# Optimization experiments

Measured on AMD Instinct MI355X. Metric: run time of the kernel, lower is better.

## Reference

```python
import jax, jax.numpy as jnp
from jax import lax
import numpy as np


def _conv3x3(x, w, b):
    # x: [B,C,H,W], w: [O,I,3,3] (OIHW), SAME padding, stride 1
    y = lax.conv_general_dilated(x, w, window_strides=(1, 1), padding='SAME',
                                 dimension_numbers=('NCHW', 'OIHW', 'NCHW'))
    return y + b[None, :, None, None]


def setup_inputs() -> dict:
    key = jax.random.key(0)
    ks = jax.random.split(key, 9)
    B, C, H, W = 4, 64, 64, 64
    wscale = 1.0 / np.sqrt(C * 9)  # keep conv outputs / attention logits sane
    x = jax.random.normal(ks[0], (B, C, H, W), dtype=jnp.float32)
    wq = jax.random.normal(ks[1], (C, C, 3, 3), dtype=jnp.float32) * wscale
    bq = jax.random.normal(ks[2], (C,), dtype=jnp.float32) * 0.1
    wk = jax.random.normal(ks[3], (C, C, 3, 3), dtype=jnp.float32) * wscale
    bk = jax.random.normal(ks[4], (C,), dtype=jnp.float32) * 0.1
    wv = jax.random.normal(ks[5], (C, C, 3, 3), dtype=jnp.float32) * wscale
    bv = jax.random.normal(ks[6], (C,), dtype=jnp.float32) * 0.1
    pos_gamma = jax.random.normal(ks[7], (1,), dtype=jnp.float32)
    chan_gamma = jax.random.normal(ks[8], (1,), dtype=jnp.float32)
    return {'x': x, 'wq': wq, 'bq': bq, 'wk': wk, 'bk': bk, 'wv': wv, 'bv': bv,
            'pos_gamma': pos_gamma, 'chan_gamma': chan_gamma}


def reference(x, wq, bq, wk, bk, wv, bv, pos_gamma, chan_gamma):
    B, C, H, W = x.shape
    N = H * W
    # position (spatial) self-attention over N = H*W locations
    q = _conv3x3(x, wq, bq).reshape(B, C, N)
    k = _conv3x3(x, wk, bk).reshape(B, C, N)
    v = _conv3x3(x, wv, bv).reshape(B, C, N)
    # attn[b,i,j] = softmax_j( sum_c q[b,c,i] * k[b,c,j] )
    pos_attn = jax.nn.softmax(jnp.einsum('bci,bcj->bij', q, k), axis=-1)
    # pos_out[b,c,j] = sum_i v[b,c,i] * attn[b,i,j]  (matches torch.bmm(v, attn))
    pos = jnp.einsum('bci,bij->bcj', v, pos_attn).reshape(B, C, H, W)
    pos_out = pos_gamma * pos + x
    # channel self-attention over C channels (x is its own q/k/v)
    xf = x.reshape(B, C, N)
    chan_attn = jax.nn.softmax(jnp.einsum('bcn,bdn->bcd', xf, xf), axis=-1)
    chan = jnp.einsum('bcd,bdn->bcn', chan_attn, xf).reshape(B, C, H, W)
    chan_out = chan_gamma * chan + x
    return pos_out + chan_out
```

## Files before the change

kernel.cpp:

```cpp
#include <hip/hip_runtime.h>

#define OFF_XV2   65536u
#define OFF_GP    589824u
#define OFF_Q2    1048576u
#define OFF_K2    2097152u
#define OFF_V2    3145728u
#define OFF_X2    3670016u
#define OFF_WT    4194304u
#define OFF_INVL  4452352u
#define OFF_A     4730880u
#define WS_FLOATS 4747264u

typedef short s8v __attribute__((ext_vector_type(8)));
typedef float f16v __attribute__((ext_vector_type(16)));

#define MFMA32(a, b, c) __builtin_amdgcn_mfma_f32_32x32x16_bf16((a), (b), (c), 0, 0, 0)

__device__ __forceinline__ unsigned short bf16_rne(float f) {
    union { float f; unsigned int u; } v; v.f = f;
    unsigned int r = v.u + 0x7FFFu + ((v.u >> 16) & 1u);
    return (unsigned short)(r >> 16);
}
__device__ __forceinline__ float bf2f(unsigned short h) {
    union { unsigned int u; float f; } t; t.u = ((unsigned int)h) << 16;
    return t.f;
}
__device__ __forceinline__ void split2(float f, unsigned short& h, unsigned short& l) {
    unsigned short hh = bf16_rne(f);
    h = hh;
    l = bf16_rne(f - bf2f(hh));
}
__device__ __forceinline__ unsigned int cvtpk(float lo, float hi) {
    unsigned int r;
    asm("v_cvt_pk_bf16_f32 %0, %1, %2" : "=v"(r) : "v"(lo), "v"(hi));
    return r;
}
__device__ __forceinline__ void pl32swap(unsigned int& a, unsigned int& b) {
    asm volatile("v_permlane32_swap_b32 %0, %1" : "+v"(a), "+v"(b));
}
__device__ __forceinline__ s8v mk8(unsigned int w0, unsigned int w1,
                                   unsigned int w2, unsigned int w3) {
    union { unsigned int u[4]; s8v v; } t;
    t.u[0] = w0; t.u[1] = w1; t.u[2] = w2; t.u[3] = w3;
    return t.v;
}
__device__ __forceinline__ f16v zero16() {
    f16v z;
#pragma unroll
    for (int i = 0; i < 16; ++i) z[i] = 0.0f;
    return z;
}


__global__ void k_wtrans(const float* __restrict__ wq, const float* __restrict__ wk,
                         const float* __restrict__ wv, unsigned short* __restrict__ wf) {
    int t = blockIdx.x * 256 + threadIdx.x;
    int f = t >> 9, pos = t & 511;
    int lane = pos >> 3, e = pos & 7;
    int oc = f & 1, kst = (f >> 1) & 3;
    int ct = f >> 3;
    int tap = ct % 9, conv = ct / 9;
    int o = oc * 32 + (lane & 31);
    int ci = kst * 16 + (lane >> 5) * 8 + e;
    const float* w = (conv == 0) ? wq : (conv == 1) ? wk : wv;
    float v = w[(o * 64 + ci) * 9 + tap];
    unsigned short hh, ll;
    split2(v, hh, ll);
    wf[(f * 2 + 0) * 512 + pos] = hh;
    wf[(f * 2 + 1) * 512 + pos] = ll;
}

__global__ __launch_bounds__(256) void k_xpack(const float* __restrict__ x,
                                               unsigned short* __restrict__ X2,
                                               unsigned short* __restrict__ XV2) {
    int gid = blockIdx.x * 256 + threadIdx.x;
    int b = gid >> 16;
    int c = (gid >> 10) & 63;
    int n4 = (gid & 1023) * 4;
    float4 v = *(const float4*)(x + (size_t)(b * 64 + c) * 4096 + n4);
    unsigned short hv[4] = {bf16_rne(v.x), bf16_rne(v.y), bf16_rne(v.z), bf16_rne(v.w)};
    int kst = c >> 4, e = c & 7, hb = (c >> 3) & 1;
#pragma unroll
    for (int u = 0; u < 4; ++u) {
        int n = n4 + u;
        int nch = n >> 5, lane = (n & 31) + 32 * hb;
        X2[(size_t)((b * 128 + nch) * 4 + kst) * 512 + lane * 8 + e] = hv[u];
    }
    int ich = n4 >> 5, ksub = (n4 >> 4) & 1, cb = c >> 5;
    int lane2 = (c & 31) + 32 * ((n4 >> 3) & 1);
    size_t xi = (size_t)(((b * 128 + ich) * 2 + ksub) * 2 + cb) * 512 + lane2 * 8 + (n4 & 7);
    unsigned long long w = (unsigned long long)hv[0]
                         | ((unsigned long long)hv[1] << 16)
                         | ((unsigned long long)hv[2] << 32)
                         | ((unsigned long long)hv[3] << 48);
    *(unsigned long long*)(XV2 + xi) = w;
}

__global__ __launch_bounds__(384) void k_conv(
        const float* __restrict__ x, const unsigned short* __restrict__ wf,
        const float* __restrict__ bq, const float* __restrict__ bk, const float* __restrict__ bv,
        unsigned short* __restrict__ Q2, unsigned short* __restrict__ K2,
        unsigned short* __restrict__ V2) {
    int nb = blockIdx.x;
    int b = blockIdx.y;
    int h = nb >> 1, w0 = (nb & 1) * 32;

    __shared__ unsigned short xwh[6528];
    __shared__ unsigned short xwl[6528];

    int tid = threadIdx.x;
    for (int idx = tid; idx < 6528; idx += 384) {
        int W = idx % 34;
        int c = (idx / 34) & 63;
        int dy = idx / (34 * 64);
        int hs = h + dy - 1, wi = w0 + W - 1;
        float v = 0.0f;
        if (hs >= 0 && hs < 64 && wi >= 0 && wi < 64)
            v = x[((b * 64 + c) * 64 + hs) * 64 + wi];
        unsigned short hh_, ll_;
        split2(v, hh_, ll_);
        int row = dy * 34 + W;
        int byt = row * 128 + c * 2;
        int swz = byt ^ ((row & 7) << 4);
        *(unsigned short*)((char*)xwh + swz) = hh_;
        *(unsigned short*)((char*)xwl + swz) = ll_;
    }
    __syncthreads();

    int lane = tid & 63, wv = tid >> 6;
    int conv = wv >> 1, oc = wv & 1;
    int hh = lane >> 5, l31 = lane & 31;

    const float* bias = (conv == 0) ? bq : (conv == 1) ? bk : bv;
    f16v D;
    if (conv < 2) {
#pragma unroll
        for (int r = 0; r < 16; ++r)
            D[r] = bias[oc * 32 + (r & 3) + 8 * (r >> 2) + 4 * hh];
    } else {
        float bvv = bias[oc * 32 + l31];
#pragma unroll
        for (int r = 0; r < 16; ++r) D[r] = bvv;
    }

#pragma unroll
    for (int tap = 0; tap < 9; ++tap) {
        int dy = tap / 3, dx = tap % 3;
#pragma unroll
        for (int kst = 0; kst < 4; ++kst) {
            int f = ((conv * 9 + tap) * 4 + kst) * 2 + oc;
            s8v Wh = *(const s8v*)(wf + (f * 2 + 0) * 512 + lane * 8);
            s8v Wl = *(const s8v*)(wf + (f * 2 + 1) * 512 + lane * 8);
            int row = dy * 34 + dx + l31;
            int byt = row * 128 + kst * 32 + hh * 16;
            int swz = byt ^ ((row & 7) << 4);
            s8v Xh = *(const s8v*)((const char*)xwh + swz);
            s8v Xl = *(const s8v*)((const char*)xwl + swz);
            if (conv < 2) {
                D = MFMA32(Wh, Xh, D);
                D = MFMA32(Wh, Xl, D);
                D = MFMA32(Wl, Xh, D);
            } else {
                D = MFMA32(Xh, Wh, D);
                D = MFMA32(Xl, Wh, D);
                D = MFMA32(Xh, Wl, D);
            }
        }
    }

    if (conv < 2) {
        unsigned short sh[16], sl[16];
#pragma unroll
        for (int r = 0; r < 16; ++r) split2(D[r], sh[r], sl[r]);
        unsigned int ah0 = sh[0] | ((unsigned int)sh[1] << 16), ah1 = sh[2] | ((unsigned int)sh[3] << 16);
        unsigned int ah2 = sh[4] | ((unsigned int)sh[5] << 16), ah3 = sh[6] | ((unsigned int)sh[7] << 16);
        pl32swap(ah0, ah2); pl32swap(ah1, ah3);
        s8v F0h = mk8(ah0, ah1, ah2, ah3);
        unsigned int al0 = sl[0] | ((unsigned int)sl[1] << 16), al1 = sl[2] | ((unsigned int)sl[3] << 16);
        unsigned int al2 = sl[4] | ((unsigned int)sl[5] << 16), al3 = sl[6] | ((unsigned int)sl[7] << 16);
        pl32swap(al0, al2); pl32swap(al1, al3);
        s8v F0l = mk8(al0, al1, al2, al3);
        unsigned int bh0 = sh[8] | ((unsigned int)sh[9] << 16), bh1 = sh[10] | ((unsigned int)sh[11] << 16);
        unsigned int bh2 = sh[12] | ((unsigned int)sh[13] << 16), bh3 = sh[14] | ((unsigned int)sh[15] << 16);
        pl32swap(bh0, bh2); pl32swap(bh1, bh3);
        s8v F1h = mk8(bh0, bh1, bh2, bh3);
        unsigned int bl0 = sl[8] | ((unsigned int)sl[9] << 16), bl1 = sl[10] | ((unsigned int)sl[11] << 16);
        unsigned int bl2 = sl[12] | ((unsigned int)sl[13] << 16), bl3 = sl[14] | ((unsigned int)sl[15] << 16);
        pl32swap(bl0, bl2); pl32swap(bl1, bl3);
        s8v F1l = mk8(bl0, bl1, bl2, bl3);
        unsigned short* dst = (conv == 0) ? Q2 : K2;
        size_t b0 = (size_t)(((b * 128 + nb) * 4 + oc * 2 + 0) * 2) * 512 + lane * 8;
        size_t b1 = (size_t)(((b * 128 + nb) * 4 + oc * 2 + 1) * 2) * 512 + lane * 8;
        *(s8v*)(dst + b0) = F0h;
        *(s8v*)(dst + b0 + 512) = F0l;
        *(s8v*)(dst + b1) = F1h;
        *(s8v*)(dst + b1 + 512) = F1l;
    } else {
        unsigned int a0 = cvtpk(D[0], D[1]),  a1 = cvtpk(D[2], D[3]);
        unsigned int a2 = cvtpk(D[4], D[5]),  a3 = cvtpk(D[6], D[7]);
        pl32swap(a0, a2); pl32swap(a1, a3);
        s8v F0h = mk8(a0, a1, a2, a3);
        unsigned int b0w = cvtpk(D[8], D[9]),  b1w = cvtpk(D[10], D[11]);
        unsigned int b2w = cvtpk(D[12], D[13]), b3w = cvtpk(D[14], D[15]);
        pl32swap(b0w, b2w); pl32swap(b1w, b3w);
        s8v F1h = mk8(b0w, b1w, b2w, b3w);
        size_t v0 = (size_t)(((b * 128 + nb) * 2 + 0) * 2 + oc) * 512 + lane * 8;
        size_t v1 = (size_t)(((b * 128 + nb) * 2 + 1) * 2 + oc) * 512 + lane * 8;
        *(s8v*)(V2 + v0) = F0h;
        *(s8v*)(V2 + v1) = F1h;
    }
}

__global__ __launch_bounds__(256) void k_gram(const unsigned short* __restrict__ XV2,
                                              float* __restrict__ Gp) {
    int kp = blockIdx.x, b = blockIdx.y;
    int tid = threadIdx.x, lane = tid & 63, wv = tid >> 6;
    int cb1 = wv & 1, cb2 = wv >> 1;
    f16v G = zero16();
#pragma unroll
    for (int t = 0; t < 8; ++t) {
        int ich = kp * 8 + t;
        const unsigned short* base = XV2 + (size_t)(b * 128 + ich) * 2048 + lane * 8;
        s8v a0 = *(const s8v*)(base + (0 * 2 + cb1) * 512);
        s8v b0 = *(const s8v*)(base + (0 * 2 + cb2) * 512);
        s8v a1 = *(const s8v*)(base + (1 * 2 + cb1) * 512);
        s8v b1 = *(const s8v*)(base + (1 * 2 + cb2) * 512);
        G = MFMA32(a0, b0, G);
        G = MFMA32(a1, b1, G);
    }
    int hh = lane >> 5, l31 = lane & 31;
#pragma unroll
    for (int r = 0; r < 16; ++r) {
        int cc = cb1 * 32 + (r & 3) + 8 * (r >> 2) + 4 * hh;
        int dd = cb2 * 32 + l31;
        Gp[(size_t)(kp * 4 + b) * 4096 + cc * 64 + dd] = G[r];
    }
}

__global__ void k_asm(const float* __restrict__ Gp, unsigned short* __restrict__ A2) {
    int row = blockIdx.x;
    int d = threadIdx.x;
    int b = row >> 6, c = row & 63;
    float g = 0.0f;
#pragma unroll
    for (int p = 0; p < 16; ++p) g += Gp[(size_t)(p * 4 + b) * 4096 + c * 64 + d];
    float mx = g;
    for (int off = 32; off >= 1; off >>= 1) mx = fmaxf(mx, __shfl_xor(mx, off, 64));
    float e = __expf(g - mx);
    float s = e;
    for (int off = 32; off >= 1; off >>= 1) s += __shfl_xor(s, off, 64);
    float a = e / s;
    int cb = c >> 5, kst = d >> 4;
    int lane2 = (c & 31) + 32 * ((d >> 3) & 1);
    A2[(size_t)((b * 2 + cb) * 4 + kst) * 512 + lane2 * 8 + (d & 7)] = bf16_rne(a);
}

__global__ __launch_bounds__(1024) void k_pass1(
        const unsigned short* __restrict__ Q2, const unsigned short* __restrict__ K2,
        float* __restrict__ invl) {
    int flat = blockIdx.x;
    int xcd = flat & 7;
    int b = xcd >> 1;
    int ich = (xcd & 1) * 64 + (flat >> 3);
    int tid = threadIdx.x, lane = tid & 63, wv = tid >> 6;

    __shared__ float lsum[16][32];

    const unsigned short* qp = Q2 + (size_t)(b * 128 + ich) * 4096 + lane * 8;
    s8v qf0 = *(const s8v*)(qp);
    s8v qf1 = *(const s8v*)(qp + 512);
    s8v qf2 = *(const s8v*)(qp + 1024);
    s8v qf3 = *(const s8v*)(qp + 1536);
    s8v qf4 = *(const s8v*)(qp + 2048);
    s8v qf5 = *(const s8v*)(qp + 2560);
    s8v qf6 = *(const s8v*)(qp + 3072);
    s8v qf7 = *(const s8v*)(qp + 3584);

    float la0 = 0.f, la1 = 0.f;
#pragma unroll 1
    for (int t = 0; t < 8; ++t) {
        int jch = wv * 8 + t;
        const unsigned short* kp = K2 + (size_t)(b * 128 + jch) * 4096 + lane * 8;
        s8v kf0 = *(const s8v*)(kp);
        s8v kf1 = *(const s8v*)(kp + 512);
        s8v kf2 = *(const s8v*)(kp + 1024);
        s8v kf3 = *(const s8v*)(kp + 1536);
        s8v kf4 = *(const s8v*)(kp + 2048);
        s8v kf5 = *(const s8v*)(kp + 2560);
        s8v kf6 = *(const s8v*)(kp + 3072);
        s8v kf7 = *(const s8v*)(kp + 3584);
        f16v Sa = zero16(), Sb = zero16();
        Sa = MFMA32(kf0, qf0, Sa);
        Sa = MFMA32(kf0, qf1, Sa);
        Sa = MFMA32(kf1, qf0, Sa);
        Sa = MFMA32(kf2, qf2, Sa);
        Sa = MFMA32(kf2, qf3, Sa);
        Sa = MFMA32(kf3, qf2, Sa);
        Sb = MFMA32(kf4, qf4, Sb);
        Sb = MFMA32(kf4, qf5, Sb);
        Sb = MFMA32(kf5, qf4, Sb);
        Sb = MFMA32(kf6, qf6, Sb);
        Sb = MFMA32(kf6, qf7, Sb);
        Sb = MFMA32(kf7, qf6, Sb);
#pragma unroll
        for (int r = 0; r < 8; ++r) la0 += __expf(Sa[r] + Sb[r]);
#pragma unroll
        for (int r = 8; r < 16; ++r) la1 += __expf(Sa[r] + Sb[r]);
    }
    float lacc = la0 + la1;
    lacc += __shfl_xor(lacc, 32);
    if (lane < 32) lsum[wv][lane] = lacc;
    __syncthreads();
    if (tid < 32) {
        float s = 0.f;
#pragma unroll
        for (int p = 0; p < 16; ++p) s += lsum[p][tid];
        invl[b * 4096 + ich * 32 + tid] = 1.0f / s;
    }
}

__global__ __launch_bounds__(256) void k_vnorm(
        unsigned short* __restrict__ V2, const float* __restrict__ invl) {
    int u = blockIdx.x * 256 + threadIdx.x;
    int lane = u & 63, ksub = (u >> 7) & 1;
    int ich = (u >> 8) & 127, b = u >> 15;
    int n0 = ich * 32 + ksub * 16 + (lane >> 5) * 8;
    size_t base = (size_t)u * 8;
    s8v vh = *(s8v*)(V2 + base);
    float4 iv0 = *(const float4*)(invl + b * 4096 + n0);
    float4 iv1 = *(const float4*)(invl + b * 4096 + n0 + 4);
    float ivv[8] = {iv0.x, iv0.y, iv0.z, iv0.w, iv1.x, iv1.y, iv1.z, iv1.w};
    s8v o;
#pragma unroll
    for (int e = 0; e < 8; ++e)
        o[e] = (short)bf16_rne(bf2f((unsigned short)vh[e]) * ivv[e]);
    *(s8v*)(V2 + base) = o;
}

__global__ __launch_bounds__(512) void k_pass2(
        const unsigned short* __restrict__ Q2, const unsigned short* __restrict__ K2,
        const unsigned short* __restrict__ V2, const unsigned short* __restrict__ X2,
        const unsigned short* __restrict__ A2, const float* __restrict__ x,
        const float* __restrict__ pg, const float* __restrict__ cg,
        float* __restrict__ out) {
    int flat = blockIdx.x;
    int xcd = flat & 7;
    int b = xcd >> 1;
    int jt = (xcd & 1) * 64 + (flat >> 3);
    int tid = threadIdx.x, lane = tid & 63, wv = tid >> 6;

    __shared__ float rlds[4][64][32];

    const unsigned short* kp = K2 + (size_t)(b * 128 + jt) * 4096 + lane * 8;
    s8v kf0 = *(const s8v*)(kp);
    s8v kf1 = *(const s8v*)(kp + 512);
    s8v kf2 = *(const s8v*)(kp + 1024);
    s8v kf3 = *(const s8v*)(kp + 1536);
    s8v kf4 = *(const s8v*)(kp + 2048);
    s8v kf5 = *(const s8v*)(kp + 2560);
    s8v kf6 = *(const s8v*)(kp + 3072);
    s8v kf7 = *(const s8v*)(kp + 3584);

    f16v O0 = zero16(), O1 = zero16();

#pragma unroll 1
    for (int t = 0; t < 16; ++t) {
        int ich = wv * 16 + t;
        const unsigned short* qp = Q2 + (size_t)(b * 128 + ich) * 4096 + lane * 8;
        s8v qf0 = *(const s8v*)(qp);
        s8v qf1 = *(const s8v*)(qp + 512);
        s8v qf2 = *(const s8v*)(qp + 1024);
        s8v qf3 = *(const s8v*)(qp + 1536);
        s8v qf4 = *(const s8v*)(qp + 2048);
        s8v qf5 = *(const s8v*)(qp + 2560);
        s8v qf6 = *(const s8v*)(qp + 3072);
        s8v qf7 = *(const s8v*)(qp + 3584);
        const unsigned short* vp = V2 + (size_t)(b * 128 + ich) * 2048 + lane * 8;
        s8v vA = *(const s8v*)(vp);
        s8v vB = *(const s8v*)(vp + 512);
        s8v vC = *(const s8v*)(vp + 1024);
        s8v vD = *(const s8v*)(vp + 1536);

        f16v Sa = zero16(), Sb = zero16();
        Sa = MFMA32(qf0, kf0, Sa);
        Sa = MFMA32(qf0, kf1, Sa);
        Sa = MFMA32(qf1, kf0, Sa);
        Sa = MFMA32(qf2, kf2, Sa);
        Sa = MFMA32(qf2, kf3, Sa);
        Sa = MFMA32(qf3, kf2, Sa);
        Sb = MFMA32(qf4, kf4, Sb);
        Sb = MFMA32(qf4, kf5, Sb);
        Sb = MFMA32(qf5, kf4, Sb);
        Sb = MFMA32(qf6, kf6, Sb);
        Sb = MFMA32(qf6, kf7, Sb);
        Sb = MFMA32(qf7, kf6, Sb);

        float p[16];
#pragma unroll
        for (int r = 0; r < 16; ++r) p[r] = __expf(Sa[r] + Sb[r]);

        unsigned int a0 = cvtpk(p[0], p[1]),  a1 = cvtpk(p[2], p[3]);
        unsigned int a2 = cvtpk(p[4], p[5]),  a3 = cvtpk(p[6], p[7]);
        pl32swap(a0, a2);
        pl32swap(a1, a3);
        s8v P0 = mk8(a0, a1, a2, a3);
        unsigned int b0 = cvtpk(p[8], p[9]),  b1 = cvtpk(p[10], p[11]);
        unsigned int b2 = cvtpk(p[12], p[13]), b3 = cvtpk(p[14], p[15]);
        pl32swap(b0, b2);
        pl32swap(b1, b3);
        s8v P1 = mk8(b0, b1, b2, b3);

        O0 = MFMA32(vA, P0, O0);
        O0 = MFMA32(vC, P1, O0);
        O1 = MFMA32(vB, P0, O1);
        O1 = MFMA32(vD, P1, O1);
    }

    int hh = lane >> 5, jj = lane & 31;
    if (wv < 4) {
#pragma unroll
        for (int r = 0; r < 16; ++r) {
            int c = (r & 3) + 8 * (r >> 2) + 4 * hh;
            rlds[wv][c][jj] = O0[r];
            rlds[wv][c + 32][jj] = O1[r];
        }
    }
    __syncthreads();
    float sums[4];
#pragma unroll
    for (int k = 0; k < 4; ++k) {
        int el = tid + k * 512;
        int c = el >> 5, j2 = el & 31;
        sums[k] = ((rlds[0][c][j2] + rlds[1][c][j2]) + rlds[2][c][j2]) + rlds[3][c][j2];
    }
    __syncthreads();
    if (wv >= 4) {
#pragma unroll
        for (int r = 0; r < 16; ++r) {
            int c = (r & 3) + 8 * (r >> 2) + 4 * hh;
            rlds[wv - 4][c][jj] = O0[r];
            rlds[wv - 4][c + 32][jj] = O1[r];
        }
    }
    __syncthreads();
#pragma unroll
    for (int k = 0; k < 4; ++k) {
        int el = tid + k * 512;
        int c = el >> 5, j2 = el & 31;
        sums[k] = ((sums[k] + rlds[0][c][j2]) + rlds[1][c][j2]) + rlds[2][c][j2];
        sums[k] += rlds[3][c][j2];
    }
    __syncthreads();
    float* sb = &rlds[0][0][0];
    if (wv < 2) {
        int cb = wv;
        f16v Dc = zero16();
#pragma unroll
        for (int kst = 0; kst < 4; ++kst) {
            s8v af = *(const s8v*)(A2 + (size_t)((b * 2 + cb) * 4 + kst) * 512 + lane * 8);
            s8v xf = *(const s8v*)(X2 + (size_t)((b * 128 + jt) * 4 + kst) * 512 + lane * 8);
            Dc = MFMA32(af, xf, Dc);
        }
#pragma unroll
        for (int r = 0; r < 16; ++r) {
            int c = cb * 32 + (r & 3) + 8 * (r >> 2) + 4 * hh;
            sb[c * 33 + jj] = Dc[r];
        }
    }
#pragma unroll
    for (int k = 0; k < 4; ++k) {
        int el = tid + k * 512;
        int c = el >> 5, j2 = el & 31;
        sb[2112 + el] = x[(size_t)(b * 64 + c) * 4096 + jt * 32 + j2];
    }
    __syncthreads();
    float pgv = pg[0], cgv = cg[0];
#pragma unroll
    for (int k = 0; k < 4; ++k) {
        int el = tid + k * 512;
        int c = el >> 5, j2 = el & 31;
        out[(size_t)(b * 64 + c) * 4096 + jt * 32 + j2] =
            pgv * sums[k] + cgv * sb[c * 33 + j2] + 2.0f * sb[2112 + el];
    }
}

extern "C" void kernel_launch(void* const* d_in, const int* in_sizes, int n_in,
                              void* d_out, int out_size, void* d_ws, size_t ws_size,
                              hipStream_t stream) {
    const float* x  = (const float*)d_in[0];
    const float* wq = (const float*)d_in[1];
    const float* bq = (const float*)d_in[2];
    const float* wk = (const float*)d_in[3];
    const float* bk = (const float*)d_in[4];
    const float* wv = (const float*)d_in[5];
    const float* bv = (const float*)d_in[6];
    const float* pg = (const float*)d_in[7];
    const float* cg = (const float*)d_in[8];
    float* out = (float*)d_out;

    if (ws_size < (size_t)WS_FLOATS * sizeof(float)) return;
    float* ws = (float*)d_ws;
    unsigned short* XV2 = (unsigned short*)(ws + OFF_XV2);
    float* Gp = ws + OFF_GP;
    unsigned short* Q2  = (unsigned short*)(ws + OFF_Q2);
    unsigned short* K2  = (unsigned short*)(ws + OFF_K2);
    unsigned short* V2  = (unsigned short*)(ws + OFF_V2);
    unsigned short* X2  = (unsigned short*)(ws + OFF_X2);
    unsigned short* wfb = (unsigned short*)(ws + OFF_WT);
    float* invl = ws + OFF_INVL;
    unsigned short* A2  = (unsigned short*)(ws + OFF_A);

    k_wtrans<<<432, 256, 0, stream>>>(wq, wk, wv, wfb);
    k_xpack<<<1024, 256, 0, stream>>>(x, X2, XV2);
    k_conv<<<dim3(128, 4), 384, 0, stream>>>(x, wfb, bq, bk, bv, Q2, K2, V2);
    k_gram<<<dim3(16, 4), 256, 0, stream>>>(XV2, Gp);
    k_asm<<<256, 64, 0, stream>>>(Gp, A2);
    k_pass1<<<512, 1024, 0, stream>>>(Q2, K2, invl);
    k_vnorm<<<512, 256, 0, stream>>>(V2, invl);
    k_pass2<<<512, 512, 0, stream>>>(Q2, K2, V2, X2, A2, x, pg, cg, out);
}
```

Baseline: 120.0 us.

## Process two row/column tiles per block in both attention passes to reuse K/Q loads

Each pass1 block now handles two query-row tiles with 512 threads, so every loaded K fragment feeds two score computations. Each pass2 block handles two output column tiles, staging their K in LDS so every Q/V load is reused twice. Grids shrink from 512 to 256 blocks and launch bounds request two blocks per CU. The cost is more registers, a longer LDS reduction epilogue and fewer blocks to spread across CUs.

Result: faster. 110.2 us (-8.1%).

```diff
diff --git a/kernel.cpp b/kernel.cpp
--- a/kernel.cpp
+++ b/kernel.cpp
@@ -255,31 +255,40 @@
     A2[(size_t)((b * 2 + cb) * 4 + kst) * 512 + lane2 * 8 + (d & 7)] = bf16_rne(a);
 }
 
-__global__ __launch_bounds__(1024) void k_pass1(
+__global__ __launch_bounds__(512, 2) void k_pass1(
         const unsigned short* __restrict__ Q2, const unsigned short* __restrict__ K2,
         float* __restrict__ invl) {
     int flat = blockIdx.x;
     int xcd = flat & 7;
     int b = xcd >> 1;
-    int ich = (xcd & 1) * 64 + (flat >> 3);
+    int ichp = (xcd & 1) * 32 + (flat >> 3);
+    int ich0 = ichp * 2;
     int tid = threadIdx.x, lane = tid & 63, wv = tid >> 6;
 
-    __shared__ float lsum[16][32];
-
-    const unsigned short* qp = Q2 + (size_t)(b * 128 + ich) * 4096 + lane * 8;
-    s8v qf0 = *(const s8v*)(qp);
-    s8v qf1 = *(const s8v*)(qp + 512);
-    s8v qf2 = *(const s8v*)(qp + 1024);
-    s8v qf3 = *(const s8v*)(qp + 1536);
-    s8v qf4 = *(const s8v*)(qp + 2048);
-    s8v qf5 = *(const s8v*)(qp + 2560);
-    s8v qf6 = *(const s8v*)(qp + 3072);
-    s8v qf7 = *(const s8v*)(qp + 3584);
-
-    float la0 = 0.f, la1 = 0.f;
+    __shared__ float lsum[8][2][32];
+
+    const unsigned short* qp = Q2 + (size_t)(b * 128 + ich0) * 4096 + lane * 8;
+    s8v q0f0 = *(const s8v*)(qp);
+    s8v q0f1 = *(const s8v*)(qp + 512);
+    s8v q0f2 = *(const s8v*)(qp + 1024);
+    s8v q0f3 = *(const s8v*)(qp + 1536);
+    s8v q0f4 = *(const s8v*)(qp + 2048);
+    s8v q0f5 = *(const s8v*)(qp + 2560);
+    s8v q0f6 = *(const s8v*)(qp + 3072);
+    s8v q0f7 = *(const s8v*)(qp + 3584);
+    s8v q1f0 = *(const s8v*)(qp + 4096);
+    s8v q1f1 = *(const s8v*)(qp + 4608);
+    s8v q1f2 = *(const s8v*)(qp + 5120);
+    s8v q1f3 = *(const s8v*)(qp + 5632);
+    s8v q1f4 = *(const s8v*)(qp + 6144);
+    s8v q1f5 = *(const s8v*)(qp + 6656);
+    s8v q1f6 = *(const s8v*)(qp + 7168);
+    s8v q1f7 = *(const s8v*)(qp + 7680);
+
+    float la0 = 0.f, la1 = 0.f, lb0 = 0.f, lb1 = 0.f;
 #pragma unroll 1
-    for (int t = 0; t < 8; ++t) {
-        int jch = wv * 8 + t;
+    for (int t = 0; t < 16; ++t) {
+        int jch = wv * 16 + t;
         const unsigned short* kp = K2 + (size_t)(b * 128 + jch) * 4096 + lane * 8;
         s8v kf0 = *(const s8v*)(kp);
         s8v kf1 = *(const s8v*)(kp + 512);
@@ -289,33 +298,60 @@
         s8v kf5 = *(const s8v*)(kp + 2560);
         s8v kf6 = *(const s8v*)(kp + 3072);
         s8v kf7 = *(const s8v*)(kp + 3584);
-        f16v Sa = zero16(), Sb = zero16();
-        Sa = MFMA32(kf0, qf0, Sa);
-        Sa = MFMA32(kf0, qf1, Sa);
-        Sa = MFMA32(kf1, qf0, Sa);
-        Sa = MFMA32(kf2, qf2, Sa);
-        Sa = MFMA32(kf2, qf3, Sa);
-        Sa = MFMA32(kf3, qf2, Sa);
-        Sb = MFMA32(kf4, qf4, Sb);
-        Sb = MFMA32(kf4, qf5, Sb);
-        Sb = MFMA32(kf5, qf4, Sb);
-        Sb = MFMA32(kf6, qf6, Sb);
-        Sb = MFMA32(kf6, qf7, Sb);
-        Sb = MFMA32(kf7, qf6, Sb);
-#pragma unroll
-        for (int r = 0; r < 8; ++r) la0 += __expf(Sa[r] + Sb[r]);
-#pragma unroll
-        for (int r = 8; r < 16; ++r) la1 += __expf(Sa[r] + Sb[r]);
-    }
-    float lacc = la0 + la1;
-    lacc += __shfl_xor(lacc, 32);
-    if (lane < 32) lsum[wv][lane] = lacc;
-    __syncthreads();
-    if (tid < 32) {
+        {
+            f16v Sa = zero16(), Sb = zero16();
+            Sa = MFMA32(kf0, q0f0, Sa);
+            Sa = MFMA32(kf0, q0f1, Sa);
+            Sa = MFMA32(kf1, q0f0, Sa);
+            Sa = MFMA32(kf2, q0f2, Sa);
+            Sa = MFMA32(kf2, q0f3, Sa);
+            Sa = MFMA32(kf3, q0f2, Sa);
+            Sb = MFMA32(kf4, q0f4, Sb);
+            Sb = MFMA32(kf4, q0f5, Sb);
+            Sb = MFMA32(kf5, q0f4, Sb);
+            Sb = MFMA32(kf6, q0f6, Sb);
+            Sb = MFMA32(kf6, q0f7, Sb);
+            Sb = MFMA32(kf7, q0f6, Sb);
+#pragma unroll
+            for (int r = 0; r < 8; ++r) la0 += __expf(Sa[r] + Sb[r]);
+#pragma unroll
+            for (int r = 8; r < 16; ++r) la1 += __expf(Sa[r] + Sb[r]);
+        }
+        {
+            f16v Sa = zero16(), Sb = zero16();
+            Sa = MFMA32(kf0, q1f0, Sa);
+            Sa = MFMA32(kf0, q1f1, Sa);
+            Sa = MFMA32(kf1, q1f0, Sa);
+            Sa = MFMA32(kf2, q1f2, Sa);
+            Sa = MFMA32(kf2, q1f3, Sa);
+            Sa = MFMA32(kf3, q1f2, Sa);
+            Sb = MFMA32(kf4, q1f4, Sb);
+            Sb = MFMA32(kf4, q1f5, Sb);
+            Sb = MFMA32(kf5, q1f4, Sb);
+            Sb = MFMA32(kf6, q1f6, Sb);
+            Sb = MFMA32(kf6, q1f7, Sb);
+            Sb = MFMA32(kf7, q1f6, Sb);
+#pragma unroll
+            for (int r = 0; r < 8; ++r) lb0 += __expf(Sa[r] + Sb[r]);
+#pragma unroll
+            for (int r = 8; r < 16; ++r) lb1 += __expf(Sa[r] + Sb[r]);
+        }
+    }
+    float lacc0 = la0 + la1;
+    lacc0 += __shfl_xor(lacc0, 32);
+    float lacc1 = lb0 + lb1;
+    lacc1 += __shfl_xor(lacc1, 32);
+    if (lane < 32) {
+        lsum[wv][0][lane] = lacc0;
+        lsum[wv][1][lane] = lacc1;
+    }
+    __syncthreads();
+    if (tid < 64) {
+        int ic = tid >> 5, iL = tid & 31;
         float s = 0.f;
 #pragma unroll
-        for (int p = 0; p < 16; ++p) s += lsum[p][tid];
-        invl[b * 4096 + ich * 32 + tid] = 1.0f / s;
+        for (int p = 0; p < 8; ++p) s += lsum[p][ic][iL];
+        invl[b * 4096 + (ich0 + ic) * 32 + iL] = 1.0f / s;
     }
 }
 
@@ -337,7 +373,7 @@
     *(s8v*)(V2 + base) = o;
 }
 
-__global__ __launch_bounds__(512) void k_pass2(
+__global__ __launch_bounds__(512, 2) void k_pass2(
         const unsigned short* __restrict__ Q2, const unsigned short* __restrict__ K2,
         const unsigned short* __restrict__ V2, const unsigned short* __restrict__ X2,
         const unsigned short* __restrict__ A2, const float* __restrict__ x,
@@ -346,22 +382,26 @@
     int flat = blockIdx.x;
     int xcd = flat & 7;
     int b = xcd >> 1;
-    int jt = (xcd & 1) * 64 + (flat >> 3);
+    int jtp = (xcd & 1) * 32 + (flat >> 3);
+    int jt0 = jtp * 2;
     int tid = threadIdx.x, lane = tid & 63, wv = tid >> 6;
 
-    __shared__ float rlds[4][64][32];
-
-    const unsigned short* kp = K2 + (size_t)(b * 128 + jt) * 4096 + lane * 8;
-    s8v kf0 = *(const s8v*)(kp);
-    s8v kf1 = *(const s8v*)(kp + 512);
-    s8v kf2 = *(const s8v*)(kp + 1024);
-    s8v kf3 = *(const s8v*)(kp + 1536);
-    s8v kf4 = *(const s8v*)(kp + 2048);
-    s8v kf5 = *(const s8v*)(kp + 2560);
-    s8v kf6 = *(const s8v*)(kp + 3072);
-    s8v kf7 = *(const s8v*)(kp + 3584);
-
-    f16v O0 = zero16(), O1 = zero16();
+    __shared__ float smem[12288];
+    unsigned short* Klds = (unsigned short*)(smem + 8192);
+    float* rl = smem;
+
+    {
+        const unsigned short* ksrc = K2 + (size_t)(b * 128 + jt0) * 4096;
+#pragma unroll
+        for (int s = 0; s < 2; ++s) {
+            int seg = tid + s * 512;
+            *(s8v*)(Klds + seg * 8) = *(const s8v*)(ksrc + seg * 8);
+        }
+    }
+    __syncthreads();
+
+    f16v O0a = zero16(), O1a = zero16();
+    f16v O0b = zero16(), O1b = zero16();
 
 #pragma unroll 1
     for (int t = 0; t < 16; ++t) {
@@ -381,106 +421,158 @@
         s8v vC = *(const s8v*)(vp + 1024);
         s8v vD = *(const s8v*)(vp + 1536);
 
-        f16v Sa = zero16(), Sb = zero16();
-        Sa = MFMA32(qf0, kf0, Sa);
-        Sa = MFMA32(qf0, kf1, Sa);
-        Sa = MFMA32(qf1, kf0, Sa);
-        Sa = MFMA32(qf2, kf2, Sa);
-        Sa = MFMA32(qf2, kf3, Sa);
-        Sa = MFMA32(qf3, kf2, Sa);
-        Sb = MFMA32(qf4, kf4, Sb);
-        Sb = MFMA32(qf4, kf5, Sb);
-        Sb = MFMA32(qf5, kf4, Sb);
-        Sb = MFMA32(qf6, kf6, Sb);
-        Sb = MFMA32(qf6, kf7, Sb);
-        Sb = MFMA32(qf7, kf6, Sb);
-
-        float p[16];
-#pragma unroll
-        for (int r = 0; r < 16; ++r) p[r] = __expf(Sa[r] + Sb[r]);
-
-        unsigned int a0 = cvtpk(p[0], p[1]),  a1 = cvtpk(p[2], p[3]);
-        unsigned int a2 = cvtpk(p[4], p[5]),  a3 = cvtpk(p[6], p[7]);
-        pl32swap(a0, a2);
-        pl32swap(a1, a3);
-        s8v P0 = mk8(a0, a1, a2, a3);
-        unsigned int b0 = cvtpk(p[8], p[9]),  b1 = cvtpk(p[10], p[11]);
-        unsigned int b2 = cvtpk(p[12], p[13]), b3 = cvtpk(p[14], p[15]);
-        pl32swap(b0, b2);
-        pl32swap(b1, b3);
-        s8v P1 = mk8(b0, b1, b2, b3);
-
-        O0 = MFMA32(vA, P0, O0);
-        O0 = MFMA32(vC, P1, O0);
-        O1 = MFMA32(vB, P0, O1);
-        O1 = MFMA32(vD, P1, O1);
+#pragma unroll
+        for (int js = 0; js < 2; ++js) {
+            const unsigned short* kl = Klds + js * 4096 + lane * 8;
+            s8v kf0 = *(const s8v*)(kl);
+            s8v kf1 = *(const s8v*)(kl + 512);
+            s8v kf2 = *(const s8v*)(kl + 1024);
+            s8v kf3 = *(const s8v*)(kl + 1536);
+            s8v kf4 = *(const s8v*)(kl + 2048);
+            s8v kf5 = *(const s8v*)(kl + 2560);
+            s8v kf6 = *(const s8v*)(kl + 3072);
+            s8v kf7 = *(const s8v*)(kl + 3584);
+
+            f16v Sa = zero16(), Sb = zero16();
+            Sa = MFMA32(qf0, kf0, Sa);
+            Sa = MFMA32(qf0, kf1, Sa);
+            Sa = MFMA32(qf1, kf0, Sa);
+            Sa = MFMA32(qf2, kf2, Sa);
+            Sa = MFMA32(qf2, kf3, Sa);
+            Sa = MFMA32(qf3, kf2, Sa);
+            Sb = MFMA32(qf4, kf4, Sb);
+            Sb = MFMA32(qf4, kf5, Sb);
+            Sb = MFMA32(qf5, kf4, Sb);
+            Sb = MFMA32(qf6, kf6, Sb);
+            Sb = MFMA32(qf6, kf7, Sb);
+            Sb = MFMA32(qf7, kf6, Sb);
+
+            float p[16];
+#pragma unroll
+            for (int r = 0; r < 16; ++r) p[r] = __expf(Sa[r] + Sb[r]);
+
+            unsigned int a0 = cvtpk(p[0], p[1]),  a1 = cvtpk(p[2], p[3]);
+            unsigned int a2 = cvtpk(p[4], p[5]),  a3 = cvtpk(p[6], p[7]);
+            pl32swap(a0, a2);
+            pl32swap(a1, a3);
+            s8v P0 = mk8(a0, a1, a2, a3);
+            unsigned int b0 = cvtpk(p[8], p[9]),  b1 = cvtpk(p[10], p[11]);
+            unsigned int b2 = cvtpk(p[12], p[13]), b3 = cvtpk(p[14], p[15]);
+            pl32swap(b0, b2);
+            pl32swap(b1, b3);
+            s8v P1 = mk8(b0, b1, b2, b3);
+
+            if (js == 0) {
+                O0a = MFMA32(vA, P0, O0a);
+                O0a = MFMA32(vC, P1, O0a);
+                O1a = MFMA32(vB, P0, O1a);
+                O1a = MFMA32(vD, P1, O1a);
+            } else {
+                O0b = MFMA32(vA, P0, O0b);
+                O0b = MFMA32(vC, P1, O0b);
+                O1b = MFMA32(vB, P0, O1b);
+                O1b = MFMA32(vD, P1, O1b);
+            }
+        }
     }
 
     int hh = lane >> 5, jj = lane & 31;
+    float s0[4], s1[4];
     if (wv < 4) {
 #pragma unroll
         for (int r = 0; r < 16; ++r) {
             int c = (r & 3) + 8 * (r >> 2) + 4 * hh;
-            rlds[wv][c][jj] = O0[r];
-            rlds[wv][c + 32][jj] = O1[r];
-        }
-    }
-    __syncthreads();
-    float sums[4];
+            rl[(wv * 64 + c) * 32 + jj] = O0a[r];
+            rl[(wv * 64 + c + 32) * 32 + jj] = O1a[r];
+        }
+    }
+    __syncthreads();
+#pragma unroll
+    for (int k = 0; k < 4; ++k) {
+        int el = tid + k * 512;
+        s0[k] = ((rl[el] + rl[2048 + el]) + rl[4096 + el]) + rl[6144 + el];
+    }
+    __syncthreads();
+    if (wv >= 4) {
+#pragma unroll
+        for (int r = 0; r < 16; ++r) {
+            int c = (r & 3) + 8 * (r >> 2) + 4 * hh;
+            rl[((wv - 4) * 64 + c) * 32 + jj] = O0a[r];
+            rl[((wv - 4) * 64 + c + 32) * 32 + jj] = O1a[r];
+        }
+    }
+    __syncthreads();
+#pragma unroll
+    for (int k = 0; k < 4; ++k) {
+        int el = tid + k * 512;
+        s0[k] = ((s0[k] + rl[el]) + rl[2048 + el]) + rl[4096 + el];
+        s0[k] += rl[6144 + el];
+    }
+    __syncthreads();
+    if (wv < 4) {
+#pragma unroll
+        for (int r = 0; r < 16; ++r) {
+            int c = (r & 3) + 8 * (r >> 2) + 4 * hh;
+            rl[(wv * 64 + c) * 32 + jj] = O0b[r];
+            rl[(wv * 64 + c + 32) * 32 + jj] = O1b[r];
+        }
+    }
+    __syncthreads();
+#pragma unroll
+    for (int k = 0; k < 4; ++k) {
+        int el = tid + k * 512;
+        s1[k] = ((rl[el] + rl[2048 + el]) + rl[4096 + el]) + rl[6144 + el];
+    }
+    __syncthreads();
+    if (wv >= 4) {
+#pragma unroll
+        for (int r = 0; r < 16; ++r) {
+            int c = (r & 3) + 8 * (r >> 2) + 4 * hh;
+            rl[((wv - 4) * 64 + c) * 32 + jj] = O0b[r];
+            rl[((wv - 4) * 64 + c + 32) * 32 + jj] = O1b[r];
+        }
+    }
+    __syncthreads();
+#pragma unroll
+    for (int k = 0; k < 4; ++k) {
+        int el = tid + k * 512;
+        s1[k] = ((s1[k] + rl[el]) + rl[2048 + el]) + rl[4096 + el];
+        s1[k] += rl[6144 + el];
+    }
+    __syncthreads();
+
+    float* chan = smem;
+    float* xres = smem + 4160;
+    if (wv < 4) {
+        int jts = wv >> 1, cb = wv & 1;
+        f16v Dc = zero16();
+#pragma unroll
+        for (int kst = 0; kst < 4; ++kst) {
+            s8v af = *(const s8v*)(A2 + (size_t)((b * 2 + cb) * 4 + kst) * 512 + lane * 8);
+            s8v xf = *(const s8v*)(X2 + (size_t)((b * 128 + jt0 + jts) * 4 + kst) * 512 + lane * 8);
+            Dc = MFMA32(af, xf, Dc);
+        }
+#pragma unroll
+        for (int r = 0; r < 16; ++r) {
+            int c = cb * 32 + (r & 3) + 8 * (r >> 2) + 4 * hh;
+            chan[c * 65 + jts * 32 + jj] = Dc[r];
+        }
+    }
+#pragma unroll
+    for (int k = 0; k < 8; ++k) {
+        int el = tid + k * 512;
+        int c = el >> 6, j2 = el & 63;
+        xres[el] = x[(size_t)(b * 64 + c) * 4096 + jtp * 64 + j2];
+    }
+    __syncthreads();
+    float pgv = pg[0], cgv = cg[0];
 #pragma unroll
     for (int k = 0; k < 4; ++k) {
         int el = tid + k * 512;
         int c = el >> 5, j2 = el & 31;
-        sums[k] = ((rlds[0][c][j2] + rlds[1][c][j2]) + rlds[2][c][j2]) + rlds[3][c][j2];
-    }
-    __syncthreads();
-    if (wv >= 4) {
-#pragma unroll
-        for (int r = 0; r < 16; ++r) {
-            int c = (r & 3) + 8 * (r >> 2) + 4 * hh;
-            rlds[wv - 4][c][jj] = O0[r];
-            rlds[wv - 4][c + 32][jj] = O1[r];
-        }
-    }
-    __syncthreads();
-#pragma unroll
-    for (int k = 0; k < 4; ++k) {
-        int el = tid + k * 512;
-        int c = el >> 5, j2 = el & 31;
-        sums[k] = ((sums[k] + rlds[0][c][j2]) + rlds[1][c][j2]) + rlds[2][c][j2];
-        sums[k] += rlds[3][c][j2];
-    }
-    __syncthreads();
-    float* sb = &rlds[0][0][0];
-    if (wv < 2) {
-        int cb = wv;
-        f16v Dc = zero16();
-#pragma unroll
-        for (int kst = 0; kst < 4; ++kst) {
-            s8v af = *(const s8v*)(A2 + (size_t)((b * 2 + cb) * 4 + kst) * 512 + lane * 8);
-            s8v xf = *(const s8v*)(X2 + (size_t)((b * 128 + jt) * 4 + kst) * 512 + lane * 8);
-            Dc = MFMA32(af, xf, Dc);
-        }
-#pragma unroll
-        for (int r = 0; r < 16; ++r) {
-            int c = cb * 32 + (r & 3) + 8 * (r >> 2) + 4 * hh;
-            sb[c * 33 + jj] = Dc[r];
-        }
-    }
-#pragma unroll
-    for (int k = 0; k < 4; ++k) {
-        int el = tid + k * 512;
-        int c = el >> 5, j2 = el & 31;
-        sb[2112 + el] = x[(size_t)(b * 64 + c) * 4096 + jt * 32 + j2];
-    }
-    __syncthreads();
-    float pgv = pg[0], cgv = cg[0];
-#pragma unroll
-    for (int k = 0; k < 4; ++k) {
-        int el = tid + k * 512;
-        int c = el >> 5, j2 = el & 31;
-        out[(size_t)(b * 64 + c) * 4096 + jt * 32 + j2] =
-            pgv * sums[k] + cgv * sb[c * 33 + j2] + 2.0f * sb[2112 + el];
+        size_t ob = (size_t)(b * 64 + c) * 4096 + jtp * 64;
+        out[ob + j2] = pgv * s0[k] + cgv * chan[c * 65 + j2] + 2.0f * xres[c * 64 + j2];
+        out[ob + 32 + j2] = pgv * s1[k] + cgv * chan[c * 65 + 32 + j2] + 2.0f * xres[c * 64 + 32 + j2];
     }
 }
 
@@ -515,7 +607,7 @@
     k_conv<<<dim3(128, 4), 384, 0, stream>>>(x, wfb, bq, bk, bv, Q2, K2, V2);
     k_gram<<<dim3(16, 4), 256, 0, stream>>>(XV2, Gp);
     k_asm<<<256, 64, 0, stream>>>(Gp, A2);
-    k_pass1<<<512, 1024, 0, stream>>>(Q2, K2, invl);
+    k_pass1<<<256, 512, 0, stream>>>(Q2, K2, invl);
     k_vnorm<<<512, 256, 0, stream>>>(V2, invl);
-    k_pass2<<<512, 512, 0, stream>>>(Q2, K2, V2, X2, A2, x, pg, cg, out);
-}
+    k_pass2<<<256, 512, 0, stream>>>(Q2, K2, V2, X2, A2, x, pg, cg, out);
+}
```
